# Performance work log

Hardware: AMD Instinct MI355X
Metric: run time of the kernel (lower is better)

Reference implementation:

```python
import jax, jax.numpy as jnp
import numpy as np

N_SRC = 50000   # e.g. users
N_DST = 50000   # e.g. items
N = N_SRC + N_DST
E = 1_600_000   # edges (avg degree ~16)
D = 64          # in_size == out_size


def _xavier(key, shape):
    # xavier_uniform for Linear(weight shape [out, in])
    fan_out, fan_in = shape
    limit = jnp.sqrt(6.0 / (fan_in + fan_out)).astype(jnp.float32)
    return jax.random.uniform(key, shape, jnp.float32, -limit, limit)


def setup_inputs() -> dict:
    key = jax.random.key(0)
    ks = jax.random.split(key, 8)
    return {
        "src_embedding": jax.random.normal(ks[0], (N_SRC, D), jnp.float32),
        "dst_embedding": jax.random.normal(ks[1], (N_DST, D), jnp.float32),
        "norm": jax.random.uniform(ks[2], (E, 1), jnp.float32),
        "W1": _xavier(ks[3], (D, D)),
        "b1": jnp.zeros((D,), jnp.float32),
        "W2": _xavier(ks[4], (D, D)),
        "b2": jnp.zeros((D,), jnp.float32),
        "edges_src": jax.random.randint(ks[5], (E,), 0, N, dtype=jnp.int32),
        "edges_dst": jax.random.randint(ks[6], (E,), 0, N, dtype=jnp.int32),
    }


def reference(src_embedding, dst_embedding, norm, W1, b1, W2, b2,
              edges_src, edges_dst):
    # concat user/item node tables: [N, D]
    x = jnp.concatenate([src_embedding, dst_embedding], axis=0)
    xs = x[edges_src]                      # [E, D] gather (edge source nodes)
    xd = x[edges_dst]                      # [E, D] gather (edge dest nodes)
    # msgs = W1(x_src) + W2(x_src * x_dst), per edge
    msgs = (jnp.einsum('ed,od->eo', xs, W1) + b1
            + jnp.einsum('ed,od->eo', xs * xd, W2) + b2)   # [E, D]
    msgs = norm * msgs                     # per-edge scalar normalization
    # copy_e + sum: scatter-sum messages onto destination nodes
    h = jax.ops.segment_sum(msgs, edges_dst, num_segments=N)  # [N, D]
    # LeakyReLU(0.2); dropout is identity in eval / p=0
    return jnp.where(h > 0, h, 0.2 * h)
```

## Files before the change

### kernel.cpp

```cpp
#include <hip/hip_runtime.h>
#include <hip/hip_bf16.h>


#define CHUNK 4096
#define NBMAX 1024
#define BCAP  2304

typedef __attribute__((ext_vector_type(8))) short short8v;
typedef __attribute__((ext_vector_type(4))) float f32x4;
union U4S8 { uint4 u; short8v s; };

__device__ __forceinline__ unsigned int f2bf(float f) {
    unsigned int u = __float_as_uint(f);
    u += 0x7fffu + ((u >> 16) & 1u);
    return u >> 16;
}
__device__ __forceinline__ unsigned int pkbf(float lo, float hi) {
    return (f2bf(hi) << 16) | f2bf(lo);
}

__global__ __launch_bounds__(256) void prep_init_kernel(
    const float* __restrict__ srcEmb, const float* __restrict__ dstEmb,
    unsigned int* __restrict__ xbf, int* __restrict__ gcur,
    int Ntot, int n_src, int NB)
{
    int i = blockIdx.x * 256 + threadIdx.x;
    if (i < NB) gcur[i] = i * BCAP;
    if (i >= Ntot * 32) return;
    int n = i >> 5, w = i & 31;
    const float* row = (n < n_src) ? srcEmb + (size_t)n * 64
                                   : dstEmb + (size_t)(n - n_src) * 64;
    xbf[i] = (f2bf(row[w + 32]) << 16) | f2bf(row[w]);
}

__global__ __launch_bounds__(1024) void part_scatter_kernel(
    const int* __restrict__ es, const int* __restrict__ ed,
    const float* __restrict__ norm, int* __restrict__ gcur,
    uint2* __restrict__ epk, int E, int NB)
{
    __shared__ int   bcnt[NBMAX];
    __shared__ int   lstart[NBMAX];
    __shared__ int   gbase[NBMAX];
    __shared__ int   sc[NBMAX];
    __shared__ uint2 sorted[CHUNK];

    int t  = threadIdx.x;
    int e0 = blockIdx.x * CHUNK;

    bcnt[t] = 0;
    __syncthreads();

    int dreg[4];
    #pragma unroll
    for (int k = 0; k < 4; ++k) {
        int e = e0 + t + k * 1024;
        dreg[k] = (e < E) ? ed[e] : -1;
        if (dreg[k] >= 0) atomicAdd(&bcnt[dreg[k] >> 7], 1);
    }
    __syncthreads();

    int c = (t < NB) ? bcnt[t] : 0;
    sc[t] = c;
    __syncthreads();
    for (int off = 1; off < NBMAX; off <<= 1) {
        int x = 0;
        if (t >= off) x = sc[t - off];
        __syncthreads();
        if (t >= off) sc[t] += x;
        __syncthreads();
    }
    int ex = sc[t] - c;
    lstart[t] = ex;
    bcnt[t]   = ex;
    if (c > 0) gbase[t] = atomicAdd(&gcur[t], c);
    __syncthreads();

    #pragma unroll
    for (int k = 0; k < 4; ++k) {
        int e = e0 + t + k * 1024;
        if (dreg[k] >= 0) {
            unsigned int q = (unsigned int)(norm[e] * 32767.f + 0.5f);
            if (q > 32767u) q = 32767u;
            int lp = atomicAdd(&bcnt[dreg[k] >> 7], 1);
            uint2 r; r.x = (unsigned int)es[e];
            r.y = ((unsigned int)dreg[k] << 15) | q;
            sorted[lp] = r;
        }
    }
    __syncthreads();

    int total = E - e0; if (total > CHUNK) total = CHUNK;
    for (int i = t; i < total; i += 1024) {
        uint2 r = sorted[i];
        int b = (int)(r.y >> 22);
        int gpos = gbase[b] + (i - lstart[b]);
        if (gpos < (b + 1) * BCAP)
            epk[gpos] = r;
    }
}

__global__ __launch_bounds__(512) void bucket_sort_kernel(
    const int* __restrict__ gcur, const uint2* __restrict__ epk,
    uint2* __restrict__ epk2, int* __restrict__ offsets2)
{
    __shared__ int bh[128];
    __shared__ int sc[128];

    int b = blockIdx.x, t = threadIdx.x;
    int base  = b * BCAP;
    int total = gcur[b] - base;
    if (total > BCAP) total = BCAP;

    if (t < 128) bh[t] = 0;
    __syncthreads();
    for (int i = t; i < total; i += 512)
        atomicAdd(&bh[(epk[base + i].y >> 15) & 127], 1);
    __syncthreads();

    int v = 0;
    if (t < 128) { v = bh[t]; sc[t] = v; }
    __syncthreads();
    for (int off = 1; off < 128; off <<= 1) {
        int x = 0;
        if (t < 128 && t >= off) x = sc[t - off];
        __syncthreads();
        if (t < 128 && t >= off) sc[t] += x;
        __syncthreads();
    }
    if (t < 128) {
        int ex = sc[t] - v;
        offsets2[b * 129 + t] = ex;
        if (t == 127) offsets2[b * 129 + 128] = sc[127];
        bh[t] = ex;
    }
    __syncthreads();

    for (int i = t; i < total; i += 512) {
        uint2 r = epk[base + i];
        int pos = atomicAdd(&bh[(r.y >> 15) & 127], 1);
        epk2[base + pos] = r;
    }
}

__global__ __launch_bounds__(256) void accumulate_kernel(
    const unsigned int* __restrict__ xbf,
    const int* __restrict__ offsets2, const uint2* __restrict__ epk2,
    unsigned int* __restrict__ Acat, float* __restrict__ cnt, int Ntot)
{
    int idx = blockIdx.x * 256 + threadIdx.x;
    int n   = idx >> 3;
    if (n >= Ntot) return;
    int sl  = threadIdx.x & 7;
    int b   = n >> 7;
    int loc = n & 127;

    int s0 = b * BCAP + offsets2[b * 129 + loc];
    int s1 = b * BCAP + offsets2[b * 129 + loc + 1];

    float ax0 = 0.f, ax1 = 0.f, ax2 = 0.f, ax3 = 0.f;
    float ay0 = 0.f, ay1 = 0.f, ay2 = 0.f, ay3 = 0.f;
    float c = 0.f;

    for (int r = s0; r < s1; r += 2) {
        uint2 p0 = epk2[r];
        int ok1  = (r + 1 < s1);
        uint2 p1 = epk2[ok1 ? r + 1 : r];
        uint4 u0 = *(const uint4*)(xbf + (size_t)p0.x * 32 + 4 * sl);
        uint4 u1 = *(const uint4*)(xbf + (size_t)p1.x * 32 + 4 * sl);
        float w0 = (float)(p0.y & 0x7fffu) * (1.f / 32767.f);
        float w1 = ok1 ? (float)(p1.y & 0x7fffu) * (1.f / 32767.f) : 0.f;
        ax0 = fmaf(w0, __uint_as_float(u0.x << 16), ax0);
        ax1 = fmaf(w0, __uint_as_float(u0.y << 16), ax1);
        ax2 = fmaf(w0, __uint_as_float(u0.z << 16), ax2);
        ax3 = fmaf(w0, __uint_as_float(u0.w << 16), ax3);
        ay0 = fmaf(w0, __uint_as_float(u0.x & 0xffff0000u), ay0);
        ay1 = fmaf(w0, __uint_as_float(u0.y & 0xffff0000u), ay1);
        ay2 = fmaf(w0, __uint_as_float(u0.z & 0xffff0000u), ay2);
        ay3 = fmaf(w0, __uint_as_float(u0.w & 0xffff0000u), ay3);
        ax0 = fmaf(w1, __uint_as_float(u1.x << 16), ax0);
        ax1 = fmaf(w1, __uint_as_float(u1.y << 16), ax1);
        ax2 = fmaf(w1, __uint_as_float(u1.z << 16), ax2);
        ax3 = fmaf(w1, __uint_as_float(u1.w << 16), ax3);
        ay0 = fmaf(w1, __uint_as_float(u1.x & 0xffff0000u), ay0);
        ay1 = fmaf(w1, __uint_as_float(u1.y & 0xffff0000u), ay1);
        ay2 = fmaf(w1, __uint_as_float(u1.z & 0xffff0000u), ay2);
        ay3 = fmaf(w1, __uint_as_float(u1.w & 0xffff0000u), ay3);
        c += w0 + w1;
    }

    uint4 xv = *(const uint4*)(xbf + (size_t)n * 32 + 4 * sl);
    float xl0 = __uint_as_float(xv.x << 16);
    float xl1 = __uint_as_float(xv.y << 16);
    float xl2 = __uint_as_float(xv.z << 16);
    float xl3 = __uint_as_float(xv.w << 16);
    float xh0 = __uint_as_float(xv.x & 0xffff0000u);
    float xh1 = __uint_as_float(xv.y & 0xffff0000u);
    float xh2 = __uint_as_float(xv.z & 0xffff0000u);
    float xh3 = __uint_as_float(xv.w & 0xffff0000u);

    uint4 w0;
    w0.x = pkbf(ax0, ax1);
    w0.y = pkbf(ax2, ax3);
    w0.z = pkbf(ay0, ay1);
    w0.w = pkbf(ay2, ay3);
    uint4 w1;
    w1.x = pkbf(ax0 * xl0, ax1 * xl1);
    w1.y = pkbf(ax2 * xl2, ax3 * xl3);
    w1.z = pkbf(ay0 * xh0, ay1 * xh1);
    w1.w = pkbf(ay2 * xh2, ay3 * xh3);
    *(uint4*)(Acat + (size_t)n * 64 + 4 * sl)      = w0;
    *(uint4*)(Acat + (size_t)n * 64 + 32 + 4 * sl) = w1;
    if (sl == 0) cnt[n] = c;
}

__global__ __launch_bounds__(256) void node_gemm_kernel(
    const unsigned int* __restrict__ Acat, const float* __restrict__ cnt,
    const float* __restrict__ W1, const float* __restrict__ b1,
    const float* __restrict__ W2, const float* __restrict__ b2,
    float* __restrict__ out, int Ntot)
{
    __shared__ unsigned int wlds[64 * 68];

    int t     = threadIdx.x;
    int lane  = t & 63;
    int wv    = t >> 6;
    int base  = blockIdx.x * 64;
    int row16 = lane & 15;
    int q     = lane >> 4;

    int arow = base + wv * 16 + row16;
    if (arow >= Ntot) arow = Ntot - 1;
    const uint4* ap = (const uint4*)(Acat + (size_t)arow * 64);
    uint4 af[4];
    #pragma unroll
    for (int s = 0; s < 4; ++s) af[s] = ap[s * 4 + q];

    for (int i = t; i < 64 * 64; i += 256) {
        int o = i >> 6, j = i & 63;
        int jj = j & 31, sl = jj >> 2, tt = jj & 3;
        int d0 = 4 * sl + ((tt & 1) << 1) + ((tt & 2) ? 32 : 0);
        const float* wsrc = (j < 32) ? W1 : W2;
        wlds[o * 68 + j] = pkbf(wsrc[o * 64 + d0], wsrc[o * 64 + d0 + 1]);
    }

    float cload[4];
    #pragma unroll
    for (int r = 0; r < 4; ++r) {
        int grow = base + wv * 16 + q * 4 + r;
        cload[r] = cnt[grow < Ntot ? grow : (Ntot - 1)];
    }
    f32x4 acc[4];
    #pragma unroll
    for (int j = 0; j < 4; ++j) {
        int col = j * 16 + row16;
        float bs = b1[col] + b2[col];
        #pragma unroll
        for (int r = 0; r < 4; ++r) acc[j][r] = cload[r] * bs;
    }
    __syncthreads();

    #pragma unroll
    for (int s = 0; s < 4; ++s) {
        U4S8 a; a.u = af[s];
        #pragma unroll
        for (int j = 0; j < 4; ++j) {
            int o = j * 16 + row16;
            U4S8 bb; bb.u = *(const uint4*)(wlds + o * 68 + s * 16 + q * 4);
            acc[j] = __builtin_amdgcn_mfma_f32_16x16x32_bf16(
                a.s, bb.s, acc[j], 0, 0, 0);
        }
    }

    #pragma unroll
    for (int r = 0; r < 4; ++r) {
        int grow = base + wv * 16 + q * 4 + r;
        if (grow < Ntot) {
            #pragma unroll
            for (int j = 0; j < 4; ++j) {
                float a = acc[j][r];
                out[(size_t)grow * 64 + j * 16 + row16] = (a > 0.f) ? a : 0.2f * a;
            }
        }
    }
}

extern "C" void kernel_launch(void* const* d_in, const int* in_sizes, int n_in,
                              void* d_out, int out_size, void* d_ws, size_t ws_size,
                              hipStream_t stream) {
    const float* srcEmb = (const float*)d_in[0];
    const float* dstEmb = (const float*)d_in[1];
    const float* norm   = (const float*)d_in[2];
    const float* W1     = (const float*)d_in[3];
    const float* b1     = (const float*)d_in[4];
    const float* W2     = (const float*)d_in[5];
    const float* b2     = (const float*)d_in[6];
    const int*   es     = (const int*)d_in[7];
    const int*   ed     = (const int*)d_in[8];

    const int n_src = in_sizes[0] / 64;
    const int n_dst = in_sizes[1] / 64;
    const int Ntot  = n_src + n_dst;
    const int E     = in_sizes[7];
    const int NB    = (Ntot + 127) >> 7;

    float* cnt      = (float*)d_ws;
    int*   gcur     = (int*)(cnt + Ntot);
    int*   offsets2 = gcur + NB;
    size_t off4     = (size_t)Ntot + NB + (size_t)NB * 129;
    off4 = (off4 + 3) & ~(size_t)3;
    uint2* epk      = (uint2*)((float*)d_ws + off4);
    uint2* epk2     = epk + (size_t)NB * BCAP;
    unsigned int* xbf = (unsigned int*)(epk2 + (size_t)NB * BCAP);
    unsigned int* Acat = (unsigned int*)d_out;

    prep_init_kernel<<<(Ntot * 32 + 255) / 256, 256, 0, stream>>>(
        srcEmb, dstEmb, xbf, gcur, Ntot, n_src, NB);

    part_scatter_kernel<<<(E + CHUNK - 1) / CHUNK, 1024, 0, stream>>>(
        es, ed, norm, gcur, epk, E, NB);

    bucket_sort_kernel<<<NB, 512, 0, stream>>>(gcur, epk, epk2, offsets2);

    accumulate_kernel<<<(Ntot * 8 + 255) / 256, 256, 0, stream>>>(
        xbf, offsets2, epk2, Acat, cnt, Ntot);

    node_gemm_kernel<<<(Ntot + 63) / 64, 256, 0, stream>>>(
        Acat, cnt, W1, b1, W2, b2, (float*)d_out, Ntot);
}
```

Measured before the change: 206.9 us.

## Fuse bucket sort into accumulation using LDS float atomics per bucket

Removes the per-bucket counting sort and the separate segmented accumulation kernel. Each block now takes one 128-node bucket, gathers source rows for its unsorted edges, and accumulates the weighted rows into a shared-memory tile with float atomics before writing the Acat and cnt outputs. This saves a full read/write pass over the edge list, an extra launch, and the offsets array. In exchange it relies on many LDS atomics and can contend when several edges in a bucket share a destination. Accumulation order also becomes nondeterministic.

```diff
diff --git a/kernel.cpp b/kernel.cpp
--- a/kernel.cpp
+++ b/kernel.cpp
@@ -99,118 +99,75 @@
     }
 }
 
-__global__ __launch_bounds__(512) void bucket_sort_kernel(
+__global__ __launch_bounds__(512) void accum_fused_kernel(
+    const unsigned int* __restrict__ xbf,
     const int* __restrict__ gcur, const uint2* __restrict__ epk,
-    uint2* __restrict__ epk2, int* __restrict__ offsets2)
-{
-    __shared__ int bh[128];
-    __shared__ int sc[128];
+    unsigned int* __restrict__ Acat, float* __restrict__ cnt, int Ntot)
+{
+    __shared__ float acc[128 * 65];
+    __shared__ float lcnt[128];
 
     int b = blockIdx.x, t = threadIdx.x;
+    for (int i = t; i < 128 * 65; i += 512) acc[i] = 0.f;
+    if (t < 128) lcnt[t] = 0.f;
+    __syncthreads();
+
     int base  = b * BCAP;
     int total = gcur[b] - base;
     if (total > BCAP) total = BCAP;
 
-    if (t < 128) bh[t] = 0;
-    __syncthreads();
-    for (int i = t; i < total; i += 512)
-        atomicAdd(&bh[(epk[base + i].y >> 15) & 127], 1);
-    __syncthreads();
-
-    int v = 0;
-    if (t < 128) { v = bh[t]; sc[t] = v; }
-    __syncthreads();
-    for (int off = 1; off < 128; off <<= 1) {
-        int x = 0;
-        if (t < 128 && t >= off) x = sc[t - off];
-        __syncthreads();
-        if (t < 128 && t >= off) sc[t] += x;
-        __syncthreads();
-    }
-    if (t < 128) {
-        int ex = sc[t] - v;
-        offsets2[b * 129 + t] = ex;
-        if (t == 127) offsets2[b * 129 + 128] = sc[127];
-        bh[t] = ex;
-    }
-    __syncthreads();
-
-    for (int i = t; i < total; i += 512) {
+    int g = t >> 3, sl = t & 7;
+    #pragma unroll 2
+    for (int i = g; i < total; i += 64) {
         uint2 r = epk[base + i];
-        int pos = atomicAdd(&bh[(r.y >> 15) & 127], 1);
-        epk2[base + pos] = r;
-    }
-}
-
-__global__ __launch_bounds__(256) void accumulate_kernel(
-    const unsigned int* __restrict__ xbf,
-    const int* __restrict__ offsets2, const uint2* __restrict__ epk2,
-    unsigned int* __restrict__ Acat, float* __restrict__ cnt, int Ntot)
-{
-    int idx = blockIdx.x * 256 + threadIdx.x;
-    int n   = idx >> 3;
-    if (n >= Ntot) return;
-    int sl  = threadIdx.x & 7;
-    int b   = n >> 7;
-    int loc = n & 127;
-
-    int s0 = b * BCAP + offsets2[b * 129 + loc];
-    int s1 = b * BCAP + offsets2[b * 129 + loc + 1];
-
-    float ax0 = 0.f, ax1 = 0.f, ax2 = 0.f, ax3 = 0.f;
-    float ay0 = 0.f, ay1 = 0.f, ay2 = 0.f, ay3 = 0.f;
-    float c = 0.f;
-
-    for (int r = s0; r < s1; r += 2) {
-        uint2 p0 = epk2[r];
-        int ok1  = (r + 1 < s1);
-        uint2 p1 = epk2[ok1 ? r + 1 : r];
-        uint4 u0 = *(const uint4*)(xbf + (size_t)p0.x * 32 + 4 * sl);
-        uint4 u1 = *(const uint4*)(xbf + (size_t)p1.x * 32 + 4 * sl);
-        float w0 = (float)(p0.y & 0x7fffu) * (1.f / 32767.f);
-        float w1 = ok1 ? (float)(p1.y & 0x7fffu) * (1.f / 32767.f) : 0.f;
-        ax0 = fmaf(w0, __uint_as_float(u0.x << 16), ax0);
-        ax1 = fmaf(w0, __uint_as_float(u0.y << 16), ax1);
-        ax2 = fmaf(w0, __uint_as_float(u0.z << 16), ax2);
-        ax3 = fmaf(w0, __uint_as_float(u0.w << 16), ax3);
-        ay0 = fmaf(w0, __uint_as_float(u0.x & 0xffff0000u), ay0);
-        ay1 = fmaf(w0, __uint_as_float(u0.y & 0xffff0000u), ay1);
-        ay2 = fmaf(w0, __uint_as_float(u0.z & 0xffff0000u), ay2);
-        ay3 = fmaf(w0, __uint_as_float(u0.w & 0xffff0000u), ay3);
-        ax0 = fmaf(w1, __uint_as_float(u1.x << 16), ax0);
-        ax1 = fmaf(w1, __uint_as_float(u1.y << 16), ax1);
-        ax2 = fmaf(w1, __uint_as_float(u1.z << 16), ax2);
-        ax3 = fmaf(w1, __uint_as_float(u1.w << 16), ax3);
-        ay0 = fmaf(w1, __uint_as_float(u1.x & 0xffff0000u), ay0);
-        ay1 = fmaf(w1, __uint_as_float(u1.y & 0xffff0000u), ay1);
-        ay2 = fmaf(w1, __uint_as_float(u1.z & 0xffff0000u), ay2);
-        ay3 = fmaf(w1, __uint_as_float(u1.w & 0xffff0000u), ay3);
-        c += w0 + w1;
-    }
-
-    uint4 xv = *(const uint4*)(xbf + (size_t)n * 32 + 4 * sl);
-    float xl0 = __uint_as_float(xv.x << 16);
-    float xl1 = __uint_as_float(xv.y << 16);
-    float xl2 = __uint_as_float(xv.z << 16);
-    float xl3 = __uint_as_float(xv.w << 16);
-    float xh0 = __uint_as_float(xv.x & 0xffff0000u);
-    float xh1 = __uint_as_float(xv.y & 0xffff0000u);
-    float xh2 = __uint_as_float(xv.z & 0xffff0000u);
-    float xh3 = __uint_as_float(xv.w & 0xffff0000u);
-
-    uint4 w0;
-    w0.x = pkbf(ax0, ax1);
-    w0.y = pkbf(ax2, ax3);
-    w0.z = pkbf(ay0, ay1);
-    w0.w = pkbf(ay2, ay3);
-    uint4 w1;
-    w1.x = pkbf(ax0 * xl0, ax1 * xl1);
-    w1.y = pkbf(ax2 * xl2, ax3 * xl3);
-    w1.z = pkbf(ay0 * xh0, ay1 * xh1);
-    w1.w = pkbf(ay2 * xh2, ay3 * xh3);
-    *(uint4*)(Acat + (size_t)n * 64 + 4 * sl)      = w0;
-    *(uint4*)(Acat + (size_t)n * 64 + 32 + 4 * sl) = w1;
-    if (sl == 0) cnt[n] = c;
+        uint4 u = *(const uint4*)(xbf + (size_t)r.x * 32 + 4 * sl);
+        float w = (float)(r.y & 0x7fffu) * (1.f / 32767.f);
+        int loc = (int)((r.y >> 15) & 127);
+        float* a = acc + loc * 65 + 4 * sl;
+        atomicAdd(a + 0,  w * __uint_as_float(u.x << 16));
+        atomicAdd(a + 1,  w * __uint_as_float(u.y << 16));
+        atomicAdd(a + 2,  w * __uint_as_float(u.z << 16));
+        atomicAdd(a + 3,  w * __uint_as_float(u.w << 16));
+        atomicAdd(a + 32, w * __uint_as_float(u.x & 0xffff0000u));
+        atomicAdd(a + 33, w * __uint_as_float(u.y & 0xffff0000u));
+        atomicAdd(a + 34, w * __uint_as_float(u.z & 0xffff0000u));
+        atomicAdd(a + 35, w * __uint_as_float(u.w & 0xffff0000u));
+        if (sl == 0) atomicAdd(&lcnt[loc], w);
+    }
+    __syncthreads();
+
+    for (int s = t; s < 1024; s += 512) {
+        int loc = s >> 3, psl = s & 7;
+        int n = b * 128 + loc;
+        if (n >= Ntot) continue;
+        const float* a = acc + loc * 65 + 4 * psl;
+        float ax0 = a[0],  ax1 = a[1],  ax2 = a[2],  ax3 = a[3];
+        float ay0 = a[32], ay1 = a[33], ay2 = a[34], ay3 = a[35];
+
+        uint4 xv = *(const uint4*)(xbf + (size_t)n * 32 + 4 * psl);
+        float xl0 = __uint_as_float(xv.x << 16);
+        float xl1 = __uint_as_float(xv.y << 16);
+        float xl2 = __uint_as_float(xv.z << 16);
+        float xl3 = __uint_as_float(xv.w << 16);
+        float xh0 = __uint_as_float(xv.x & 0xffff0000u);
+        float xh1 = __uint_as_float(xv.y & 0xffff0000u);
+        float xh2 = __uint_as_float(xv.z & 0xffff0000u);
+        float xh3 = __uint_as_float(xv.w & 0xffff0000u);
+
+        uint4 w0;
+        w0.x = pkbf(ax0, ax1);
+        w0.y = pkbf(ax2, ax3);
+        w0.z = pkbf(ay0, ay1);
+        w0.w = pkbf(ay2, ay3);
+        uint4 w1;
+        w1.x = pkbf(ax0 * xl0, ax1 * xl1);
+        w1.y = pkbf(ax2 * xl2, ax3 * xl3);
+        w1.z = pkbf(ay0 * xh0, ay1 * xh1);
+        w1.w = pkbf(ay2 * xh2, ay3 * xh3);
+        *(uint4*)(Acat + (size_t)n * 64 + 4 * psl)      = w0;
+        *(uint4*)(Acat + (size_t)n * 64 + 32 + 4 * psl) = w1;
+        if (psl == 0) cnt[n] = lcnt[loc];
+    }
 }
 
 __global__ __launch_bounds__(256) void node_gemm_kernel(
@@ -305,12 +262,10 @@
 
     float* cnt      = (float*)d_ws;
     int*   gcur     = (int*)(cnt + Ntot);
-    int*   offsets2 = gcur + NB;
-    size_t off4     = (size_t)Ntot + NB + (size_t)NB * 129;
+    size_t off4     = (size_t)Ntot + NB;
     off4 = (off4 + 3) & ~(size_t)3;
     uint2* epk      = (uint2*)((float*)d_ws + off4);
-    uint2* epk2     = epk + (size_t)NB * BCAP;
-    unsigned int* xbf = (unsigned int*)(epk2 + (size_t)NB * BCAP);
+    unsigned int* xbf = (unsigned int*)(epk + (size_t)NB * BCAP);
     unsigned int* Acat = (unsigned int*)d_out;
 
     prep_init_kernel<<<(Ntot * 32 + 255) / 256, 256, 0, stream>>>(
@@ -319,10 +274,8 @@
     part_scatter_kernel<<<(E + CHUNK - 1) / CHUNK, 1024, 0, stream>>>(
         es, ed, norm, gcur, epk, E, NB);
 
-    bucket_sort_kernel<<<NB, 512, 0, stream>>>(gcur, epk, epk2, offsets2);
-
-    accumulate_kernel<<<(Ntot * 8 + 255) / 256, 256, 0, stream>>>(
-        xbf, offsets2, epk2, Acat, cnt, Ntot);
+    accum_fused_kernel<<<NB, 512, 0, stream>>>(
+        xbf, gcur, epk, Acat, cnt, Ntot);
 
     node_gemm_kernel<<<(Ntot + 63) / 64, 256, 0, stream>>>(
         Acat, cnt, W1, b1, W2, b2, (float*)d_out, Ntot);
```

Result: slower. 827.3 us (+299.9%).
